# Kernel optimization log

Hardware: AMD Instinct MI355X
Metric: run time of the kernel (lower is better)

Reference implementation:

```python
import jax, jax.numpy as jnp
import numpy as np

N = 50000
E = 1600000
VOCAB = 1000
EMB = 128
HID = 128
OUT = 128


def setup_inputs() -> dict:
    key = jax.random.key(0)
    ks = jax.random.split(key, 8)
    labels = jax.random.randint(ks[0], (N,), 0, VOCAB)
    edge_index = jax.random.randint(ks[1], (2, E), 0, N)
    weight = jax.random.uniform(ks[2], (E,), dtype=jnp.float32)
    emb_table = jax.random.normal(ks[3], (VOCAB, EMB), dtype=jnp.float32) * 0.02
    W1 = jax.random.normal(ks[4], (EMB, HID), dtype=jnp.float32) * (1.0 / np.sqrt(EMB))
    b1 = jnp.zeros((HID,), dtype=jnp.float32)
    W2 = jax.random.normal(ks[5], (HID, OUT), dtype=jnp.float32) * (1.0 / np.sqrt(HID))
    b2 = jnp.zeros((OUT,), dtype=jnp.float32)
    return {"labels": labels, "edge_index": edge_index, "weight": weight,
            "emb_table": emb_table, "W1": W1, "b1": b1, "W2": W2, "b2": b2}


def _gcn_conv(x, src, dst, ew, W, b, n_nodes):
    # PyG GCNConv: linear transform, then symmetric-normalized weighted aggregation.
    x = x @ W  # [N, F_out]
    deg = jax.ops.segment_sum(ew, dst, num_segments=n_nodes)  # weighted in-degree (incl. self loops)
    dinv = jnp.where(deg > 0, jax.lax.rsqrt(deg), 0.0)
    norm = dinv[src] * ew * dinv[dst]  # [E_tot]
    msg = x[src] * norm[:, None]  # gather + scale
    out = jax.ops.segment_sum(msg, dst, num_segments=n_nodes)  # scatter-add
    return out + b


def reference(labels, edge_index, weight, emb_table, W1, b1, W2, b2):
    n_nodes = emb_table.shape[0] if False else labels.shape[0]
    # add self loops with weight 1.0 (GCNConv default add_self_loops=True)
    loop = jnp.arange(n_nodes, dtype=edge_index.dtype)
    src = jnp.concatenate([edge_index[0], loop])
    dst = jnp.concatenate([edge_index[1], loop])
    ew = jnp.concatenate([weight.astype(jnp.float32), jnp.ones((n_nodes,), jnp.float32)])

    x = emb_table[labels]  # embedding lookup [N, EMB]
    x = _gcn_conv(x, src, dst, ew, W1, b1, n_nodes)
    x = jax.nn.relu(x)
    x = _gcn_conv(x, src, dst, ew, W2, b2, n_nodes)
    return x
```

## Files before the change

### kernel.cpp

```cpp
#include <hip/hip_runtime.h>
#include <hip/hip_fp16.h>


#define CHUNKS 896

__global__ __launch_bounds__(256) void hist_kernel(const int* __restrict__ dst,
                                                   int* __restrict__ hist,
                                                   int e, int chunk, int nb) {
  __shared__ unsigned lh[1024];
  int b = blockIdx.x, t = threadIdx.x;
  int start = b * chunk, end = min(e, start + chunk);
  for (int i = t; i < nb; i += 256) lh[i] = 0;
  __syncthreads();
  for (int i = start + t; i < end; i += 256) atomicAdd(&lh[dst[i] >> 6], 1u);
  __syncthreads();
  for (int k = t; k < nb; k += 256) hist[(size_t)k * CHUNKS + b] = (int)lh[k];
}

__global__ __launch_bounds__(256) void colscan_kernel(const int* __restrict__ hist,
                                                      int* __restrict__ off,
                                                      int* __restrict__ tot,
                                                      int nb, int bact) {
  int k = (blockIdx.x * 256 + threadIdx.x) >> 6;
  int lane = threadIdx.x & 63;
  if (k >= nb) return;
  int carry = 0;
  for (int r = 0; r < CHUNKS / 64; ++r) {
    int b = r * 64 + lane;
    int h = (b < bact) ? hist[(size_t)k * CHUNKS + b] : 0;
    int x = h;
#pragma unroll
    for (int d = 1; d < 64; d <<= 1) {
      int tt = __shfl_up(x, d, 64);
      if (lane >= d) x += tt;
    }
    if (b < bact) off[(size_t)k * CHUNKS + b] = carry + x - h;
    carry += __shfl(x, 63, 64);
  }
  if (lane == 0) tot[k] = carry;
}

__global__ __launch_bounds__(1024) void ebase_kernel(const int* __restrict__ tot,
                                                     int* __restrict__ ebase, int nb) {
  __shared__ int wsum[16];
  int t = threadIdx.x, lane = t & 63, wv = t >> 6;
  int v = (t < nb) ? tot[t] : 0;
  int x = v;
#pragma unroll
  for (int d = 1; d < 64; d <<= 1) {
    int tt = __shfl_up(x, d, 64);
    if (lane >= d) x += tt;
  }
  if (lane == 63) wsum[wv] = x;
  __syncthreads();
  int o = 0;
#pragma unroll
  for (int w = 0; w < 16; ++w) o += (w < wv) ? wsum[w] : 0;
  int excl = x - v + o;
  if (t < nb) ebase[t] = excl;
  if (t == nb - 1) ebase[nb] = excl + v;
}

__global__ __launch_bounds__(256) void scatter_kernel(
    const int* __restrict__ src, const int* __restrict__ dst,
    const float* __restrict__ w, const int* __restrict__ labels,
    const int* __restrict__ off, const int* __restrict__ ebase,
    int2* __restrict__ brec, int e, int chunk) {
  __shared__ unsigned bincnt[1024];
  int b = blockIdx.x, t = threadIdx.x;
  int start = b * chunk, end = min(e, start + chunk);
  for (int i = t; i < 1024; i += 256) bincnt[i] = 0;
  __syncthreads();
  int s[7], d[7], lb[7], bs[7];
  float wv[7];
#pragma unroll
  for (int u = 0; u < 7; ++u) {
    int i = start + u * 256 + t;
    bool ok = i < end;
    s[u] = ok ? src[i] : 0;
    d[u] = ok ? dst[i] : 0;
    wv[u] = ok ? w[i] : 0.f;
  }
#pragma unroll
  for (int u = 0; u < 7; ++u) lb[u] = labels[s[u]];
#pragma unroll
  for (int u = 0; u < 7; ++u) {
    int k = d[u] >> 6;
    bs[u] = ebase[k] + off[(size_t)k * CHUNKS + b];
  }
#pragma unroll
  for (int u = 0; u < 7; ++u) {
    int i = start + u * 256 + t;
    if (i < end) {
      int k = d[u] >> 6;
      unsigned lr = atomicAdd(&bincnt[k], 1u);
      unsigned rx = (unsigned)s[u] | ((unsigned)(d[u] & 63) << 16) |
                    ((unsigned)lb[u] << 22);
      brec[bs[u] + (int)lr] = make_int2((int)rx, __float_as_int(wv[u]));
    }
  }
}

__global__ __launch_bounds__(256) void bsort_kernel(const int2* __restrict__ brec,
                                                    const int* __restrict__ ebase,
                                                    int2* __restrict__ csr,
                                                    int* __restrict__ rs,
                                                    float* __restrict__ dinv, int n) {
  __shared__ unsigned h64[64];
  __shared__ unsigned cur[64];
  __shared__ float rsum[64];
  int k = blockIdx.x, t = threadIdx.x;
  int e0 = ebase[k], e1 = ebase[k + 1];
  if (t < 64) { h64[t] = 0; rsum[t] = 0.f; }
  __syncthreads();
  for (int i = e0 + t; i < e1; i += 256) {
    int2 r = brec[i];
    unsigned dl = ((unsigned)r.x >> 16) & 63u;
    atomicAdd(&h64[dl], 1u);
    atomicAdd(&rsum[dl], __int_as_float(r.y));
  }
  __syncthreads();
  if (t < 64) {
    int hv = (int)h64[t];
    int x = hv;
#pragma unroll
    for (int d = 1; d < 64; d <<= 1) {
      int tt = __shfl_up(x, d, 64);
      if (t >= d) x += tt;
    }
    int ex = x - hv;
    cur[t] = (unsigned)(e0 + ex);
    int v = k * 64 + t;
    if (v <= n) rs[v] = e0 + ex;
    if (v < n) dinv[v] = rsqrtf(1.0f + rsum[t]);
  }
  __syncthreads();
  for (int i = e0 + t; i < e1; i += 256) {
    int2 r = brec[i];
    unsigned rx = (unsigned)r.x;
    int dl = (int)((rx >> 16) & 63u);
    int pos = (int)atomicAdd(&cur[dl], 1u);
    csr[pos] = make_int2((int)((rx & 0xffffu) | ((rx >> 22) << 16)), r.y);
  }
}

__global__ void temb_kernel(const float* __restrict__ emb, const float* __restrict__ W1,
                            __half* __restrict__ temb) {
  int r = blockIdx.x, j = threadIdx.x;
  __shared__ float xs[128];
  xs[j] = emb[r * 128 + j];
  __syncthreads();
  float acc = 0.f;
#pragma unroll 8
  for (int k = 0; k < 128; ++k) acc = fmaf(xs[k], W1[k * 128 + j], acc);
  temb[r * 128 + j] = __float2half_rn(acc);
}

__global__ __launch_bounds__(256) void agg1_kernel(
    const int* __restrict__ rs, const int2* __restrict__ csr,
    const float* __restrict__ dinv, const int* __restrict__ labels,
    const __half2* __restrict__ temb, const float* __restrict__ b1,
    __half2* __restrict__ out1, int n) {
  int wid = (blockIdx.x * blockDim.x + threadIdx.x) >> 6;
  int lane = threadIdx.x & 63;
  if (wid >= n) return;
  float di = dinv[wid];
  int selfrow = labels[wid];
  float2 hv = __half22float2(temb[(size_t)selfrow * 64 + lane]);
  float acc0 = hv.x * di, acc1 = hv.y * di;
  int r1v = rs[wid + 1];
  for (int base = rs[wid]; base < r1v; base += 64) {
    int s = 0;
    float v = 0.f;
    if (base + lane < r1v) {
      int2 c = csr[base + lane];
      s = c.x;
      v = __int_as_float(c.y) * dinv[c.x & 0xffff];
    }
    int nb = min(64, r1v - base);
    int j = 0;
    for (; j + 8 <= nb; j += 8) {
#pragma unroll
      for (int u = 0; u < 8; ++u) {
        int sj = __shfl(s, j + u, 64);
        float vj = __shfl(v, j + u, 64);
        float2 hs = __half22float2(temb[(size_t)(sj >> 16) * 64 + lane]);
        acc0 = fmaf(hs.x, vj, acc0);
        acc1 = fmaf(hs.y, vj, acc1);
      }
    }
    for (; j < nb; ++j) {
      int sj = __shfl(s, j, 64);
      float vj = __shfl(v, j, 64);
      float2 hs = __half22float2(temb[(size_t)(sj >> 16) * 64 + lane]);
      acc0 = fmaf(hs.x, vj, acc0);
      acc1 = fmaf(hs.y, vj, acc1);
    }
  }
  acc0 = fmaf(acc0, di, b1[2 * lane]);
  acc1 = fmaf(acc1, di, b1[2 * lane + 1]);
  out1[(size_t)wid * 64 + lane] =
      __float22half2_rn(make_float2(fmaxf(acc0, 0.f), fmaxf(acc1, 0.f)));
}

__global__ __launch_bounds__(256) void agg2_kernel(
    const int* __restrict__ rs, const int2* __restrict__ csr,
    const float* __restrict__ dinv, const __half2* __restrict__ h,
    float* __restrict__ out, int n) {
  int wid = (blockIdx.x * blockDim.x + threadIdx.x) >> 6;
  int lane = threadIdx.x & 63;
  if (wid >= n) return;
  float di = dinv[wid];
  float2 hv = __half22float2(h[(size_t)wid * 64 + lane]);
  float acc0 = hv.x * di, acc1 = hv.y * di;
  int r1v = rs[wid + 1];
  for (int base = rs[wid]; base < r1v; base += 64) {
    int s = 0;
    float v = 0.f;
    if (base + lane < r1v) {
      int2 c = csr[base + lane];
      s = c.x;
      v = __int_as_float(c.y) * dinv[c.x & 0xffff];
    }
    int nb = min(64, r1v - base);
    int j = 0;
    for (; j + 16 <= nb; j += 16) {
#pragma unroll
      for (int u = 0; u < 16; ++u) {
        int sj = __shfl(s, j + u, 64);
        float vj = __shfl(v, j + u, 64);
        float2 hs = __half22float2(h[(size_t)(sj & 0xffff) * 64 + lane]);
        acc0 = fmaf(hs.x, vj, acc0);
        acc1 = fmaf(hs.y, vj, acc1);
      }
    }
    for (; j + 8 <= nb; j += 8) {
#pragma unroll
      for (int u = 0; u < 8; ++u) {
        int sj = __shfl(s, j + u, 64);
        float vj = __shfl(v, j + u, 64);
        float2 hs = __half22float2(h[(size_t)(sj & 0xffff) * 64 + lane]);
        acc0 = fmaf(hs.x, vj, acc0);
        acc1 = fmaf(hs.y, vj, acc1);
      }
    }
    for (; j < nb; ++j) {
      int sj = __shfl(s, j, 64);
      float vj = __shfl(v, j, 64);
      float2 hs = __half22float2(h[(size_t)(sj & 0xffff) * 64 + lane]);
      acc0 = fmaf(hs.x, vj, acc0);
      acc1 = fmaf(hs.y, vj, acc1);
    }
  }
  *(float2*)(out + (size_t)wid * 128 + 2 * lane) = make_float2(acc0 * di, acc1 * di);
}

__global__ __launch_bounds__(256) void gemm_bias_kernel(float* __restrict__ y,
                                                        const float* __restrict__ W,
                                                        const float* __restrict__ bias,
                                                        int n) {
  __shared__ float xs[32][128];
  int tid = threadIdx.x;
  int tc = tid & 31;
  int tr = tid >> 5;
  int rb = blockIdx.x * 32;
  {
    const float4* xg = (const float4*)(y + (size_t)rb * 128);
    float4* xls = (float4*)&xs[0][0];
#pragma unroll
    for (int i = 0; i < 4; ++i) {
      int idx = tid + i * 256;
      int row = rb + (idx >> 5);
      float4 val = (row < n) ? xg[idx] : make_float4(0.f, 0.f, 0.f, 0.f);
      xls[idx] = val;
    }
  }
  __syncthreads();
  int j0 = tc * 4;
  float4 b4 = *(const float4*)(bias + j0);
  float acc[4][4];
#pragma unroll
  for (int r = 0; r < 4; ++r) {
    acc[r][0] = b4.x; acc[r][1] = b4.y; acc[r][2] = b4.z; acc[r][3] = b4.w;
  }
#pragma unroll 4
  for (int k = 0; k < 128; ++k) {
    float4 w4 = *(const float4*)(W + k * 128 + j0);
#pragma unroll
    for (int r = 0; r < 4; ++r) {
      float xv = xs[tr * 4 + r][k];
      acc[r][0] = fmaf(xv, w4.x, acc[r][0]);
      acc[r][1] = fmaf(xv, w4.y, acc[r][1]);
      acc[r][2] = fmaf(xv, w4.z, acc[r][2]);
      acc[r][3] = fmaf(xv, w4.w, acc[r][3]);
    }
  }
#pragma unroll
  for (int r = 0; r < 4; ++r) {
    int row = rb + tr * 4 + r;
    if (row < n)
      *(float4*)(y + (size_t)row * 128 + j0) =
          make_float4(acc[r][0], acc[r][1], acc[r][2], acc[r][3]);
  }
}

extern "C" void kernel_launch(void* const* d_in, const int* in_sizes, int n_in,
                              void* d_out, int out_size, void* d_ws, size_t ws_size,
                              hipStream_t stream) {
  const int* labels = (const int*)d_in[0];
  const int* edge_index = (const int*)d_in[1];
  const float* weight = (const float*)d_in[2];
  const float* emb = (const float*)d_in[3];
  const float* W1 = (const float*)d_in[4];
  const float* b1 = (const float*)d_in[5];
  const float* W2 = (const float*)d_in[6];
  const float* b2 = (const float*)d_in[7];

  int n = in_sizes[0];
  int e = in_sizes[1] / 2;
  int vocab = in_sizes[3] / 128;
  const int* srcp = edge_index;
  const int* dstp = edge_index + e;

  int nb = (n + 63) >> 6;
  int chunk = (e + CHUNKS - 1) / CHUNKS;
  int bact = (e + chunk - 1) / chunk;

  float* ws = (float*)d_ws;
  size_t o = 0;
  auto alloc_f = [&](size_t c) { float* p = ws + o; o += (c + 255) & ~(size_t)255; return p; };
  int*     hist  = (int*)alloc_f((size_t)nb * CHUNKS);
  int*     off   = (int*)alloc_f((size_t)nb * CHUNKS);
  int*     tot   = (int*)alloc_f(nb);
  int*     ebase = (int*)alloc_f(nb + 1);
  int2*    brec  = (int2*)alloc_f((size_t)e * 2);
  int*     rs    = (int*)alloc_f(n + 1);
  int2*    csr   = (int2*)alloc_f((size_t)e * 2);
  float*   dinv  = alloc_f(n);
  __half*  temb  = (__half*)alloc_f((size_t)vocab * 64);
  __half2* out1  = (__half2*)alloc_f((size_t)n * 64);
  (void)ws_size;

  dim3 b256(256);
  int gagg = (int)(((size_t)n * 64 + 255) / 256);

  hist_kernel<<<bact, b256, 0, stream>>>(dstp, hist, e, chunk, nb);
  colscan_kernel<<<(nb * 64 + 255) / 256, b256, 0, stream>>>(hist, off, tot, nb, bact);
  ebase_kernel<<<1, 1024, 0, stream>>>(tot, ebase, nb);
  scatter_kernel<<<bact, b256, 0, stream>>>(srcp, dstp, weight, labels, off, ebase,
                                            brec, e, chunk);
  bsort_kernel<<<nb, b256, 0, stream>>>(brec, ebase, csr, rs, dinv, n);
  temb_kernel<<<vocab, 128, 0, stream>>>(emb, W1, temb);
  agg1_kernel<<<gagg, b256, 0, stream>>>(rs, csr, dinv, labels, (const __half2*)temb,
                                         b1, out1, n);
  agg2_kernel<<<gagg, b256, 0, stream>>>(rs, csr, dinv, out1, (float*)d_out, n);
  gemm_bias_kernel<<<(n + 31) / 32, b256, 0, stream>>>((float*)d_out, W2, b2, n);
}
```

Baseline: 206.0 us.

## Split wavefront into two half-waves each gathering a different neighbor row

The aggregation kernels now have each 32-lane half of a wavefront process a different neighbor. Each lane loads 8 bytes (4 halves) per row instead of 4 bytes, and the two halves are combined with a cross-half shuffle reduction at the end. The goal is more gather memory requests in flight and fewer shuffle/loop iterations per edge. Separately, the chunk count for the edge bucketing pass drops from 896 to 256, with the scatter kernel looping over multiple 1792-edge batches per block. That cuts histogram/offset table size and scan work, at the cost of less parallelism in the hist and scatter passes.

```diff
diff --git a/kernel.cpp b/kernel.cpp
--- a/kernel.cpp
+++ b/kernel.cpp
@@ -2,7 +2,7 @@
 #include <hip/hip_fp16.h>
 
 
-#define CHUNKS 896
+#define CHUNKS 256
 
 __global__ __launch_bounds__(256) void hist_kernel(const int* __restrict__ dst,
                                                    int* __restrict__ hist,
@@ -71,32 +71,35 @@
   int start = b * chunk, end = min(e, start + chunk);
   for (int i = t; i < 1024; i += 256) bincnt[i] = 0;
   __syncthreads();
-  int s[7], d[7], lb[7], bs[7];
-  float wv[7];
-#pragma unroll
-  for (int u = 0; u < 7; ++u) {
-    int i = start + u * 256 + t;
-    bool ok = i < end;
-    s[u] = ok ? src[i] : 0;
-    d[u] = ok ? dst[i] : 0;
-    wv[u] = ok ? w[i] : 0.f;
-  }
-#pragma unroll
-  for (int u = 0; u < 7; ++u) lb[u] = labels[s[u]];
-#pragma unroll
-  for (int u = 0; u < 7; ++u) {
-    int k = d[u] >> 6;
-    bs[u] = ebase[k] + off[(size_t)k * CHUNKS + b];
-  }
-#pragma unroll
-  for (int u = 0; u < 7; ++u) {
-    int i = start + u * 256 + t;
-    if (i < end) {
+  for (int bs0 = start; bs0 < end; bs0 += 1792) {
+    int bend = min(end, bs0 + 1792);
+    int s[7], d[7], lb[7], ps[7];
+    float wv[7];
+#pragma unroll
+    for (int u = 0; u < 7; ++u) {
+      int i = bs0 + u * 256 + t;
+      bool ok = i < bend;
+      s[u] = ok ? src[i] : 0;
+      d[u] = ok ? dst[i] : 0;
+      wv[u] = ok ? w[i] : 0.f;
+    }
+#pragma unroll
+    for (int u = 0; u < 7; ++u) lb[u] = labels[s[u]];
+#pragma unroll
+    for (int u = 0; u < 7; ++u) {
       int k = d[u] >> 6;
-      unsigned lr = atomicAdd(&bincnt[k], 1u);
-      unsigned rx = (unsigned)s[u] | ((unsigned)(d[u] & 63) << 16) |
-                    ((unsigned)lb[u] << 22);
-      brec[bs[u] + (int)lr] = make_int2((int)rx, __float_as_int(wv[u]));
+      ps[u] = ebase[k] + off[(size_t)k * CHUNKS + b];
+    }
+#pragma unroll
+    for (int u = 0; u < 7; ++u) {
+      int i = bs0 + u * 256 + t;
+      if (i < bend) {
+        int k = d[u] >> 6;
+        unsigned lr = atomicAdd(&bincnt[k], 1u);
+        unsigned rx = (unsigned)s[u] | ((unsigned)(d[u] & 63) << 16) |
+                      ((unsigned)lb[u] << 22);
+        brec[ps[u] + (int)lr] = make_int2((int)rx, __float_as_int(wv[u]));
+      }
     }
   }
 }
@@ -156,18 +159,33 @@
   temb[r * 128 + j] = __float2half_rn(acc);
 }
 
+__device__ __forceinline__ void unpack4(float2 raw, float2& a, float2& b) {
+  union { float f; __half2 h; } u0, u1;
+  u0.f = raw.x;
+  u1.f = raw.y;
+  a = __half22float2(u0.h);
+  b = __half22float2(u1.h);
+}
+
 __global__ __launch_bounds__(256) void agg1_kernel(
     const int* __restrict__ rs, const int2* __restrict__ csr,
     const float* __restrict__ dinv, const int* __restrict__ labels,
-    const __half2* __restrict__ temb, const float* __restrict__ b1,
-    __half2* __restrict__ out1, int n) {
+    const __half* __restrict__ temb, const float* __restrict__ b1,
+    __half* __restrict__ out1, int n) {
   int wid = (blockIdx.x * blockDim.x + threadIdx.x) >> 6;
   int lane = threadIdx.x & 63;
   if (wid >= n) return;
+  int half = lane >> 5, fl = lane & 31;
   float di = dinv[wid];
-  int selfrow = labels[wid];
-  float2 hv = __half22float2(temb[(size_t)selfrow * 64 + lane]);
-  float acc0 = hv.x * di, acc1 = hv.y * di;
+  float acc0, acc1, acc2, acc3;
+  {
+    int selfrow = labels[wid];
+    float2 raw = ((const float2*)(temb + (size_t)selfrow * 128))[fl];
+    float2 a, b;
+    unpack4(raw, a, b);
+    float ss = half ? 0.f : di;
+    acc0 = a.x * ss; acc1 = a.y * ss; acc2 = b.x * ss; acc3 = b.y * ss;
+  }
   int r1v = rs[wid + 1];
   for (int base = rs[wid]; base < r1v; base += 64) {
     int s = 0;
@@ -179,40 +197,74 @@
     }
     int nb = min(64, r1v - base);
     int j = 0;
-    for (; j + 8 <= nb; j += 8) {
+    for (; j + 16 <= nb; j += 16) {
 #pragma unroll
       for (int u = 0; u < 8; ++u) {
-        int sj = __shfl(s, j + u, 64);
-        float vj = __shfl(v, j + u, 64);
-        float2 hs = __half22float2(temb[(size_t)(sj >> 16) * 64 + lane]);
-        acc0 = fmaf(hs.x, vj, acc0);
-        acc1 = fmaf(hs.y, vj, acc1);
+        int jj = j + 2 * u + half;
+        int sj = __shfl(s, jj, 64);
+        float vj = __shfl(v, jj, 64);
+        float2 raw = ((const float2*)(temb + (size_t)(sj >> 16) * 128))[fl];
+        float2 a, b;
+        unpack4(raw, a, b);
+        acc0 = fmaf(a.x, vj, acc0); acc1 = fmaf(a.y, vj, acc1);
+        acc2 = fmaf(b.x, vj, acc2); acc3 = fmaf(b.y, vj, acc3);
       }
     }
-    for (; j < nb; ++j) {
+    for (; j + 2 <= nb; j += 2) {
+      int jj = j + half;
+      int sj = __shfl(s, jj, 64);
+      float vj = __shfl(v, jj, 64);
+      float2 raw = ((const float2*)(temb + (size_t)(sj >> 16) * 128))[fl];
+      float2 a, b;
+      unpack4(raw, a, b);
+      acc0 = fmaf(a.x, vj, acc0); acc1 = fmaf(a.y, vj, acc1);
+      acc2 = fmaf(b.x, vj, acc2); acc3 = fmaf(b.y, vj, acc3);
+    }
+    if (j < nb) {
       int sj = __shfl(s, j, 64);
-      float vj = __shfl(v, j, 64);
-      float2 hs = __half22float2(temb[(size_t)(sj >> 16) * 64 + lane]);
-      acc0 = fmaf(hs.x, vj, acc0);
-      acc1 = fmaf(hs.y, vj, acc1);
-    }
-  }
-  acc0 = fmaf(acc0, di, b1[2 * lane]);
-  acc1 = fmaf(acc1, di, b1[2 * lane + 1]);
-  out1[(size_t)wid * 64 + lane] =
-      __float22half2_rn(make_float2(fmaxf(acc0, 0.f), fmaxf(acc1, 0.f)));
+      float vj0 = __shfl(v, j, 64);
+      float vj = half ? 0.f : vj0;
+      float2 raw = ((const float2*)(temb + (size_t)(sj >> 16) * 128))[fl];
+      float2 a, b;
+      unpack4(raw, a, b);
+      acc0 = fmaf(a.x, vj, acc0); acc1 = fmaf(a.y, vj, acc1);
+      acc2 = fmaf(b.x, vj, acc2); acc3 = fmaf(b.y, vj, acc3);
+    }
+  }
+  acc0 += __shfl_xor(acc0, 32, 64);
+  acc1 += __shfl_xor(acc1, 32, 64);
+  acc2 += __shfl_xor(acc2, 32, 64);
+  acc3 += __shfl_xor(acc3, 32, 64);
+  if (half == 0) {
+    float4 b4 = ((const float4*)b1)[fl];
+    acc0 = fmaxf(fmaf(acc0, di, b4.x), 0.f);
+    acc1 = fmaxf(fmaf(acc1, di, b4.y), 0.f);
+    acc2 = fmaxf(fmaf(acc2, di, b4.z), 0.f);
+    acc3 = fmaxf(fmaf(acc3, di, b4.w), 0.f);
+    union { float2 f2; __half2 h2[2]; } o;
+    o.h2[0] = __float22half2_rn(make_float2(acc0, acc1));
+    o.h2[1] = __float22half2_rn(make_float2(acc2, acc3));
+    ((float2*)(out1 + (size_t)wid * 128))[fl] = o.f2;
+  }
 }
 
 __global__ __launch_bounds__(256) void agg2_kernel(
     const int* __restrict__ rs, const int2* __restrict__ csr,
-    const float* __restrict__ dinv, const __half2* __restrict__ h,
+    const float* __restrict__ dinv, const __half* __restrict__ h,
     float* __restrict__ out, int n) {
   int wid = (blockIdx.x * blockDim.x + threadIdx.x) >> 6;
   int lane = threadIdx.x & 63;
   if (wid >= n) return;
+  int half = lane >> 5, fl = lane & 31;
   float di = dinv[wid];
-  float2 hv = __half22float2(h[(size_t)wid * 64 + lane]);
-  float acc0 = hv.x * di, acc1 = hv.y * di;
+  float acc0, acc1, acc2, acc3;
+  {
+    float2 raw = ((const float2*)(h + (size_t)wid * 128))[fl];
+    float2 a, b;
+    unpack4(raw, a, b);
+    float ss = half ? 0.f : di;
+    acc0 = a.x * ss; acc1 = a.y * ss; acc2 = b.x * ss; acc3 = b.y * ss;
+  }
   int r1v = rs[wid + 1];
   for (int base = rs[wid]; base < r1v; base += 64) {
     int s = 0;
@@ -226,33 +278,46 @@
     int j = 0;
     for (; j + 16 <= nb; j += 16) {
 #pragma unroll
-      for (int u = 0; u < 16; ++u) {
-        int sj = __shfl(s, j + u, 64);
-        float vj = __shfl(v, j + u, 64);
-        float2 hs = __half22float2(h[(size_t)(sj & 0xffff) * 64 + lane]);
-        acc0 = fmaf(hs.x, vj, acc0);
-        acc1 = fmaf(hs.y, vj, acc1);
+      for (int u = 0; u < 8; ++u) {
+        int jj = j + 2 * u + half;
+        int sj = __shfl(s, jj, 64);
+        float vj = __shfl(v, jj, 64);
+        float2 raw = ((const float2*)(h + (size_t)(sj & 0xffff) * 128))[fl];
+        float2 a, b;
+        unpack4(raw, a, b);
+        acc0 = fmaf(a.x, vj, acc0); acc1 = fmaf(a.y, vj, acc1);
+        acc2 = fmaf(b.x, vj, acc2); acc3 = fmaf(b.y, vj, acc3);
       }
     }
-    for (; j + 8 <= nb; j += 8) {
-#pragma unroll
-      for (int u = 0; u < 8; ++u) {
-        int sj = __shfl(s, j + u, 64);
-        float vj = __shfl(v, j + u, 64);
-        float2 hs = __half22float2(h[(size_t)(sj & 0xffff) * 64 + lane]);
-        acc0 = fmaf(hs.x, vj, acc0);
-        acc1 = fmaf(hs.y, vj, acc1);
-      }
-    }
-    for (; j < nb; ++j) {
+    for (; j + 2 <= nb; j += 2) {
+      int jj = j + half;
+      int sj = __shfl(s, jj, 64);
+      float vj = __shfl(v, jj, 64);
+      float2 raw = ((const float2*)(h + (size_t)(sj & 0xffff) * 128))[fl];
+      float2 a, b;
+      unpack4(raw, a, b);
+      acc0 = fmaf(a.x, vj, acc0); acc1 = fmaf(a.y, vj, acc1);
+      acc2 = fmaf(b.x, vj, acc2); acc3 = fmaf(b.y, vj, acc3);
+    }
+    if (j < nb) {
       int sj = __shfl(s, j, 64);
-      float vj = __shfl(v, j, 64);
-      float2 hs = __half22float2(h[(size_t)(sj & 0xffff) * 64 + lane]);
-      acc0 = fmaf(hs.x, vj, acc0);
-      acc1 = fmaf(hs.y, vj, acc1);
-    }
-  }
-  *(float2*)(out + (size_t)wid * 128 + 2 * lane) = make_float2(acc0 * di, acc1 * di);
+      float vj0 = __shfl(v, j, 64);
+      float vj = half ? 0.f : vj0;
+      float2 raw = ((const float2*)(h + (size_t)(sj & 0xffff) * 128))[fl];
+      float2 a, b;
+      unpack4(raw, a, b);
+      acc0 = fmaf(a.x, vj, acc0); acc1 = fmaf(a.y, vj, acc1);
+      acc2 = fmaf(b.x, vj, acc2); acc3 = fmaf(b.y, vj, acc3);
+    }
+  }
+  acc0 += __shfl_xor(acc0, 32, 64);
+  acc1 += __shfl_xor(acc1, 32, 64);
+  acc2 += __shfl_xor(acc2, 32, 64);
+  acc3 += __shfl_xor(acc3, 32, 64);
+  if (half == 0) {
+    ((float4*)(out + (size_t)wid * 128))[fl] =
+        make_float4(acc0 * di, acc1 * di, acc2 * di, acc3 * di);
+  }
 }
 
 __global__ __launch_bounds__(256) void gemm_bias_kernel(float* __restrict__ y,
@@ -329,16 +394,16 @@
   float* ws = (float*)d_ws;
   size_t o = 0;
   auto alloc_f = [&](size_t c) { float* p = ws + o; o += (c + 255) & ~(size_t)255; return p; };
-  int*     hist  = (int*)alloc_f((size_t)nb * CHUNKS);
-  int*     off   = (int*)alloc_f((size_t)nb * CHUNKS);
-  int*     tot   = (int*)alloc_f(nb);
-  int*     ebase = (int*)alloc_f(nb + 1);
-  int2*    brec  = (int2*)alloc_f((size_t)e * 2);
-  int*     rs    = (int*)alloc_f(n + 1);
-  int2*    csr   = (int2*)alloc_f((size_t)e * 2);
-  float*   dinv  = alloc_f(n);
-  __half*  temb  = (__half*)alloc_f((size_t)vocab * 64);
-  __half2* out1  = (__half2*)alloc_f((size_t)n * 64);
+  int*    hist  = (int*)alloc_f((size_t)nb * CHUNKS);
+  int*    off   = (int*)alloc_f((size_t)nb * CHUNKS);
+  int*    tot   = (int*)alloc_f(nb);
+  int*    ebase = (int*)alloc_f(nb + 1);
+  int2*   brec  = (int2*)alloc_f((size_t)e * 2);
+  int*    rs    = (int*)alloc_f(n + 1);
+  int2*   csr   = (int2*)alloc_f((size_t)e * 2);
+  float*  dinv  = alloc_f(n);
+  __half* temb  = (__half*)alloc_f((size_t)vocab * 64);
+  __half* out1  = (__half*)alloc_f((size_t)n * 64);
   (void)ws_size;
 
   dim3 b256(256);
@@ -351,8 +416,7 @@
                                             brec, e, chunk);
   bsort_kernel<<<nb, b256, 0, stream>>>(brec, ebase, csr, rs, dinv, n);
   temb_kernel<<<vocab, 128, 0, stream>>>(emb, W1, temb);
-  agg1_kernel<<<gagg, b256, 0, stream>>>(rs, csr, dinv, labels, (const __half2*)temb,
-                                         b1, out1, n);
+  agg1_kernel<<<gagg, b256, 0, stream>>>(rs, csr, dinv, labels, temb, b1, out1, n);
   agg2_kernel<<<gagg, b256, 0, stream>>>(rs, csr, dinv, out1, (float*)d_out, n);
   gemm_bias_kernel<<<(n + 31) / 32, b256, 0, stream>>>((float*)d_out, W2, b2, n);
 }
```

Result: faster. 200.5 us (-2.7%).
